# Performance work log

Measured on AMD Instinct MI355X. Metric: run time of the kernel, lower is better.

## Reference

```python
import jax, jax.numpy as jnp
import numpy as np


def setup_inputs() -> dict:
    key = jax.random.key(0)
    k1, k2 = jax.random.split(key)
    B, H, L = 8, 768, 4096
    x = jax.random.normal(k1, (B, H, L), dtype=jnp.float32)
    k = jax.random.normal(k2, (H, L), dtype=jnp.float32)
    return {"x": x, "k": k, "n": L}


def reference(x, k, n):
    # FFT-based long convolution: fft(x) * fft(k), inverse fft, real part,
    # truncated to the input sequence length. Inputs are real, so rfft/irfft
    # compute the identical result to complex fft + .real, at half the work.
    L = x.shape[-1]
    xf = jnp.fft.rfft(x, n=n)                 # [B, H, n//2+1] complex
    kf = jnp.fft.rfft(k, n=n)                 # [H, n//2+1]   complex
    y = jnp.fft.irfft(xf * kf, n=n)[..., :L]  # [B, H, L]
    return y.astype(x.dtype)
```

## Files before the change

### kernel.cpp

```cpp
#include <hip/hip_runtime.h>
#include <math.h>


#define NT 512
#define KF_LD 2049
#define C_SQRT1_2 0.70710678118654752f
#define INV_4096 2.44140625e-4f

#define SW(a) ((a) ^ (((a) >> 5) & 31) ^ (((a) >> 2) & 24))
__device__ __forceinline__ int WP(int a) {
  const int s = SW(a);
  return 2 * s - (s & 63);
}

__device__ __forceinline__ void sincos_rev(float f, float& sn, float& cs) {
  float s_, c_;
  asm("v_sin_f32 %0, %1" : "=v"(s_) : "v"(f));
  asm("v_cos_f32 %0, %1" : "=v"(c_) : "v"(f));
  sn = s_; cs = c_;
}

template <int SIGN>
__device__ __forceinline__ void bf8(const float ar[8], const float ai[8],
                                    float br[8], float bi[8]) {
  float s0r = ar[0] + ar[4], s0i = ai[0] + ai[4];
  float s1r = ar[0] - ar[4], s1i = ai[0] - ai[4];
  float s2r = ar[2] + ar[6], s2i = ai[2] + ai[6];
  float s3r = ar[2] - ar[6], s3i = ai[2] - ai[6];
  float E0r = s0r + s2r, E0i = s0i + s2i;
  float E2r = s0r - s2r, E2i = s0i - s2i;
  float E1r, E1i, E3r, E3i;
  if (SIGN < 0) { E1r = s1r + s3i; E1i = s1i - s3r; E3r = s1r - s3i; E3i = s1i + s3r; }
  else          { E1r = s1r - s3i; E1i = s1i + s3r; E3r = s1r + s3i; E3i = s1i - s3r; }
  float u0r = ar[1] + ar[5], u0i = ai[1] + ai[5];
  float u1r = ar[1] - ar[5], u1i = ai[1] - ai[5];
  float u2r = ar[3] + ar[7], u2i = ai[3] + ai[7];
  float u3r = ar[3] - ar[7], u3i = ai[3] - ai[7];
  float O0r = u0r + u2r, O0i = u0i + u2i;
  float O2r = u0r - u2r, O2i = u0i - u2i;
  float O1r, O1i, O3r, O3i;
  if (SIGN < 0) { O1r = u1r + u3i; O1i = u1i - u3r; O3r = u1r - u3i; O3i = u1i + u3r; }
  else          { O1r = u1r - u3i; O1i = u1i + u3r; O3r = u1r + u3i; O3i = u1i - u3r; }
  float t1r, t1i, t2r, t2i, t3r, t3i;
  if (SIGN < 0) {
    t1r = C_SQRT1_2 * (O1r + O1i); t1i = C_SQRT1_2 * (O1i - O1r);
    t2r = O2i;  t2i = -O2r;
    t3r = C_SQRT1_2 * (O3i - O3r); t3i = -C_SQRT1_2 * (O3r + O3i);
  } else {
    t1r = C_SQRT1_2 * (O1r - O1i); t1i = C_SQRT1_2 * (O1i + O1r);
    t2r = -O2i; t2i = O2r;
    t3r = -C_SQRT1_2 * (O3r + O3i); t3i = C_SQRT1_2 * (O3r - O3i);
  }
  br[0] = E0r + O0r; bi[0] = E0i + O0i;
  br[4] = E0r - O0r; bi[4] = E0i - O0i;
  br[1] = E1r + t1r; bi[1] = E1i + t1i;
  br[5] = E1r - t1r; bi[5] = E1i - t1i;
  br[2] = E2r + t2r; bi[2] = E2i + t2i;
  br[6] = E2r - t2r; bi[6] = E2i - t2i;
  br[3] = E3r + t3r; bi[3] = E3i + t3i;
  br[7] = E3r - t3r; bi[7] = E3i - t3i;
}

template <int SIGN, int S>
__device__ __forceinline__ void tw_write(float* Y, int ob,
                                         const float br[8], const float bi[8],
                                         float f1) {
  { const int i0 = WP(ob); Y[i0] = br[0]; Y[i0 + 64] = bi[0]; }
  float sn, cs;
  sincos_rev(f1, sn, cs);
  const float w1r = cs, w1i = (SIGN > 0) ? sn : -sn;
  float cwr = w1r, cwi = w1i;
#pragma unroll
  for (int m = 1; m < 8; ++m) {
    const int idx = WP(ob + S * m);
    Y[idx] = br[m] * cwr - bi[m] * cwi;
    Y[idx + 64] = br[m] * cwi + bi[m] * cwr;
    if (m < 7) {
      const float nr = cwr * w1r - cwi * w1i;
      const float ni = cwr * w1i + cwi * w1r;
      cwr = nr; cwi = ni;
    }
  }
}

template <int SIGN, int S>
__device__ __forceinline__ void stage_r8(const float* X, float* Y,
                                         const int rd[8]) {
  const int t = (int)threadIdx.x;
  const int q = t & (S - 1);
  const int p = t / S;
  float ar[8], ai[8];
#pragma unroll
  for (int j = 0; j < 8; ++j) {
    ar[j] = X[rd[j]];
    ai[j] = X[rd[j] + 64];
  }
  float br[8], bi[8];
  bf8<SIGN>(ar, ai, br, bi);
  tw_write<SIGN, S>(Y, q + 8 * S * p, br, bi, (float)(S * p) * INV_4096);
}

__device__ __forceinline__ void stage1_conv(const float* __restrict__ x0,
                                            const float* __restrict__ x1,
                                            float* Y) {
  const int t = (int)threadIdx.x;
  float ar[8], ai[8];
#pragma unroll
  for (int j = 0; j < 8; ++j) {
    ar[j] = x0[t + 512 * j];
    ai[j] = x1[t + 512 * j];
  }
  float br[8], bi[8];
  bf8<-1>(ar, ai, br, bi);
  tw_write<-1, 1>(Y, 8 * t, br, bi, (float)t * INV_4096);
}

__device__ __forceinline__ void stage4_kf(const float* X, float* Y,
                                          const float2* __restrict__ kfrow,
                                          const int rd[8]) {
  const int t = (int)threadIdx.x;
  float ar[8], ai[8];
#pragma unroll
  for (int j = 0; j < 8; ++j) {
    ar[j] = X[rd[j]];
    ai[j] = X[rd[j] + 64];
  }
  float br[8], bi[8];
  bf8<-1>(ar, ai, br, bi);
#pragma unroll
  for (int m = 0; m < 8; ++m) {
    const int k = t + 512 * m;
    float2 kv;
    if (m <= 3) {
      kv = kfrow[k];
    } else {
      kv = kfrow[4096 - k];
      kv.y = -kv.y;
    }
    const int i = WP(k);
    Y[i] = br[m] * kv.x - bi[m] * kv.y;
    Y[i + 64] = br[m] * kv.y + bi[m] * kv.x;
  }
}

__device__ __forceinline__ void stage4_store(const float* X,
                                             float* __restrict__ y0,
                                             float* __restrict__ y1,
                                             const int rd[8]) {
  const int t = (int)threadIdx.x;
  float ar[8], ai[8];
#pragma unroll
  for (int j = 0; j < 8; ++j) {
    ar[j] = X[rd[j]];
    ai[j] = X[rd[j] + 64];
  }
  float br[8], bi[8];
  bf8<1>(ar, ai, br, bi);
#pragma unroll
  for (int m = 0; m < 8; ++m) {
    const int k = t + 512 * m;
    y0[k] = br[m];
    y1[k] = bi[m];
  }
}

__device__ __forceinline__ void stage1_k(const float* __restrict__ kin,
                                         float* Y) {
  const int t = (int)threadIdx.x;
  float ar[8], ai[8];
#pragma unroll
  for (int j = 0; j < 8; ++j) {
    ar[j] = kin[t + 512 * j];
    ai[j] = 0.0f;
  }
  float br[8], bi[8];
  bf8<-1>(ar, ai, br, bi);
  tw_write<-1, 1>(Y, 8 * t, br, bi, (float)t * INV_4096);
}

__device__ __forceinline__ void stage4_kstore(const float* X,
                                              float2* __restrict__ kfrow,
                                              const int rd[8]) {
  const int t = (int)threadIdx.x;
  float ar[8], ai[8];
#pragma unroll
  for (int j = 0; j < 8; ++j) {
    ar[j] = X[rd[j]];
    ai[j] = X[rd[j] + 64];
  }
  float br[8], bi[8];
  bf8<-1>(ar, ai, br, bi);
  const float sc = 1.0f / 4096.0f;
#pragma unroll
  for (int m = 0; m < 4; ++m) {
    const int k = t + 512 * m;
    kfrow[k] = make_float2(br[m] * sc, bi[m] * sc);
  }
  if (t == 0) kfrow[2048] = make_float2(br[4] * sc, bi[4] * sc);
}

__global__ __launch_bounds__(NT) void kfft_kernel(const float* __restrict__ kin,
                                                  float2* __restrict__ kf) {
  __shared__ float A_[8192];
  __shared__ float B_[8192];
  const int t = (int)threadIdx.x;
  const int h = (int)blockIdx.x;
  int rd[8];
#pragma unroll
  for (int j = 0; j < 8; ++j) rd[j] = WP(t + 512 * j);
  stage1_k(kin + (size_t)h * 4096, A_);
  __syncthreads();
  stage_r8<-1, 8>(A_, B_, rd);
  __syncthreads();
  stage_r8<-1, 64>(B_, A_, rd);
  __syncthreads();
  stage4_kstore(A_, kf + (size_t)h * KF_LD, rd);
}

__global__ __launch_bounds__(NT) void conv_kernel(const float* __restrict__ x,
                                                  const float2* __restrict__ kf,
                                                  float* __restrict__ y, int H) {
  __shared__ float A_[8192];
  __shared__ float B_[8192];
  const int bi = (int)blockIdx.x;
  const int h = bi % H;
  const int j = bi / H;
  const size_t r0 = (size_t)(2 * j) * H + h;
  const size_t r1 = r0 + H;
  const float* src0 = x + r0 * 4096;
  const float* src1 = x + r1 * 4096;
  float* dst0 = y + r0 * 4096;
  float* dst1 = y + r1 * 4096;
  const float2* kfrow = kf + (size_t)h * KF_LD;
  const int t = (int)threadIdx.x;
  int rd[8];
#pragma unroll
  for (int jj = 0; jj < 8; ++jj) rd[jj] = WP(t + 512 * jj);
  stage1_conv(src0, src1, A_);
  __syncthreads();
  stage_r8<-1, 8>(A_, B_, rd);
  __syncthreads();
  stage_r8<-1, 64>(B_, A_, rd);
  __syncthreads();
  stage4_kf(A_, B_, kfrow, rd);
  __syncthreads();
  stage_r8<1, 1>(B_, A_, rd);
  __syncthreads();
  stage_r8<1, 8>(A_, B_, rd);
  __syncthreads();
  stage_r8<1, 64>(B_, A_, rd);
  __syncthreads();
  stage4_store(A_, dst0, dst1, rd);
}

extern "C" void kernel_launch(void* const* d_in, const int* in_sizes, int n_in,
                              void* d_out, int out_size, void* d_ws, size_t ws_size,
                              hipStream_t stream) {
  const float* x = (const float*)d_in[0];
  const float* kin = (const float*)d_in[1];
  float* y = (float*)d_out;
  const int H = in_sizes[1] / 4096;
  const int BH = in_sizes[0] / 4096;
  float2* kf = (float2*)d_ws;
  hipLaunchKernelGGL(kfft_kernel, dim3(H), dim3(NT), 0, stream, kin, kf);
  hipLaunchKernelGGL(conv_kernel, dim3(BH / 2), dim3(NT), 0, stream, x, kf, y, H);
}
```

Baseline: 62.74 us.

## Make conv blocks persistent over several pairs with register prefetch of next input

Each conv block now handles NPB=6 row pairs in sequence. While the current pair runs its FFT stages, the block prefetches the next pair's inputs into registers, so global load latency overlaps with shared-memory compute. The kernel-FFT kernel switches to a single in-place shared buffer with extra barriers, which cuts its LDS footprint. The cost is fewer blocks (pairs/6), extra register pressure, and a grid that truncates if the pair count is not divisible by 6.

Result: slower. 76.31 us (+21.6%).

```diff
diff --git a/kernel.cpp b/kernel.cpp
--- a/kernel.cpp
+++ b/kernel.cpp
@@ -3,6 +3,7 @@
 
 
 #define NT 512
+#define NPB 6
 #define KF_LD 2049
 #define C_SQRT1_2 0.70710678118654752f
 #define INV_4096 2.44140625e-4f
@@ -100,21 +101,6 @@
   tw_write<SIGN, S>(Y, q + 8 * S * p, br, bi, (float)(S * p) * INV_4096);
 }
 
-__device__ __forceinline__ void stage1_conv(const float* __restrict__ x0,
-                                            const float* __restrict__ x1,
-                                            float* Y) {
-  const int t = (int)threadIdx.x;
-  float ar[8], ai[8];
-#pragma unroll
-  for (int j = 0; j < 8; ++j) {
-    ar[j] = x0[t + 512 * j];
-    ai[j] = x1[t + 512 * j];
-  }
-  float br[8], bi[8];
-  bf8<-1>(ar, ai, br, bi);
-  tw_write<-1, 1>(Y, 8 * t, br, bi, (float)t * INV_4096);
-}
-
 __device__ __forceinline__ void stage4_kf(const float* X, float* Y,
                                           const float2* __restrict__ kfrow,
                                           const int rd[8]) {
@@ -137,7 +123,7 @@
       kv = kfrow[4096 - k];
       kv.y = -kv.y;
     }
-    const int i = WP(k);
+    const int i = rd[m];
     Y[i] = br[m] * kv.x - bi[m] * kv.y;
     Y[i + 64] = br[m] * kv.y + bi[m] * kv.x;
   }
@@ -164,93 +150,130 @@
   }
 }
 
-__device__ __forceinline__ void stage1_k(const float* __restrict__ kin,
-                                         float* Y) {
-  const int t = (int)threadIdx.x;
-  float ar[8], ai[8];
-#pragma unroll
-  for (int j = 0; j < 8; ++j) {
-    ar[j] = kin[t + 512 * j];
-    ai[j] = 0.0f;
-  }
+__device__ __forceinline__ void conv_pair(const float* __restrict__ x,
+                                          float* __restrict__ y,
+                                          const float2* __restrict__ kf,
+                                          int H, int p, int pmax,
+                                          float (&arC)[8], float (&aiC)[8],
+                                          float (&arN)[8], float (&aiN)[8],
+                                          float* A_, float* B_,
+                                          const int rd[8]) {
+  const int t = (int)threadIdx.x;
+  const int h = p % H, b2 = p / H;
+  const size_t r0 = ((size_t)(2 * b2) * H + (size_t)h) * 4096;
+  float* d0 = y + r0;
+  float* d1 = d0 + (size_t)H * 4096;
+  const float2* kfrow = kf + (size_t)h * KF_LD;
+  {
+    float br[8], bi[8];
+    bf8<-1>(arC, aiC, br, bi);
+    tw_write<-1, 1>(A_, 8 * t, br, bi, (float)t * INV_4096);
+  }
+  __syncthreads();
+  {
+    const int pn = (p + 1 < pmax) ? p + 1 : p;
+    const int hn = pn % H, bn = pn / H;
+    const float* s0 = x + ((size_t)(2 * bn) * H + (size_t)hn) * 4096;
+    const float* s1 = s0 + (size_t)H * 4096;
+#pragma unroll
+    for (int j = 0; j < 8; ++j) {
+      arN[j] = s0[t + 512 * j];
+      aiN[j] = s1[t + 512 * j];
+    }
+  }
+  stage_r8<-1, 8>(A_, B_, rd);   __syncthreads();
+  stage_r8<-1, 64>(B_, A_, rd);  __syncthreads();
+  stage4_kf(A_, B_, kfrow, rd);  __syncthreads();
+  stage_r8<1, 1>(B_, A_, rd);    __syncthreads();
+  stage_r8<1, 8>(A_, B_, rd);    __syncthreads();
+  stage_r8<1, 64>(B_, A_, rd);   __syncthreads();
+  stage4_store(A_, d0, d1, rd);
+  __syncthreads();
+}
+
+__device__ __forceinline__ void stage_r8_ip_k(float* Z, const int rd[8],
+                                              int S_, int dummy);
+template <int S>
+__device__ __forceinline__ void stage_r8_ip(float* Z, const int rd[8]) {
+  const int t = (int)threadIdx.x;
+  const int q = t & (S - 1);
+  const int p = t / S;
+  float ar[8], ai[8];
+#pragma unroll
+  for (int j = 0; j < 8; ++j) {
+    ar[j] = Z[rd[j]];
+    ai[j] = Z[rd[j] + 64];
+  }
+  __syncthreads();
   float br[8], bi[8];
   bf8<-1>(ar, ai, br, bi);
-  tw_write<-1, 1>(Y, 8 * t, br, bi, (float)t * INV_4096);
-}
-
-__device__ __forceinline__ void stage4_kstore(const float* X,
-                                              float2* __restrict__ kfrow,
-                                              const int rd[8]) {
-  const int t = (int)threadIdx.x;
-  float ar[8], ai[8];
-#pragma unroll
-  for (int j = 0; j < 8; ++j) {
-    ar[j] = X[rd[j]];
-    ai[j] = X[rd[j] + 64];
-  }
-  float br[8], bi[8];
-  bf8<-1>(ar, ai, br, bi);
-  const float sc = 1.0f / 4096.0f;
-#pragma unroll
-  for (int m = 0; m < 4; ++m) {
-    const int k = t + 512 * m;
-    kfrow[k] = make_float2(br[m] * sc, bi[m] * sc);
-  }
-  if (t == 0) kfrow[2048] = make_float2(br[4] * sc, bi[4] * sc);
+  tw_write<-1, S>(Z, q + 8 * S * p, br, bi, (float)(S * p) * INV_4096);
+  __syncthreads();
 }
 
 __global__ __launch_bounds__(NT) void kfft_kernel(const float* __restrict__ kin,
                                                   float2* __restrict__ kf) {
+  __shared__ float Z_[8192];
+  const int t = (int)threadIdx.x;
+  const int h = (int)blockIdx.x;
+  int rd[8];
+#pragma unroll
+  for (int j = 0; j < 8; ++j) rd[j] = WP(t + 512 * j);
+  {
+    const float* src = kin + (size_t)h * 4096;
+    float ar[8], ai[8];
+#pragma unroll
+    for (int j = 0; j < 8; ++j) { ar[j] = src[t + 512 * j]; ai[j] = 0.0f; }
+    float br[8], bi[8];
+    bf8<-1>(ar, ai, br, bi);
+    tw_write<-1, 1>(Z_, 8 * t, br, bi, (float)t * INV_4096);
+  }
+  __syncthreads();
+  stage_r8_ip<8>(Z_, rd);
+  stage_r8_ip<64>(Z_, rd);
+  {
+    float ar[8], ai[8];
+#pragma unroll
+    for (int j = 0; j < 8; ++j) { ar[j] = Z_[rd[j]]; ai[j] = Z_[rd[j] + 64]; }
+    float br[8], bi[8];
+    bf8<-1>(ar, ai, br, bi);
+    const float sc = 1.0f / 4096.0f;
+    float2* kfrow = kf + (size_t)h * KF_LD;
+#pragma unroll
+    for (int m = 0; m < 4; ++m) {
+      const int k = t + 512 * m;
+      kfrow[k] = make_float2(br[m] * sc, bi[m] * sc);
+    }
+    if (t == 0) kfrow[2048] = make_float2(br[4] * sc, bi[4] * sc);
+  }
+}
+
+__global__ __launch_bounds__(NT) void conv_kernel(const float* __restrict__ x,
+                                                  const float2* __restrict__ kf,
+                                                  float* __restrict__ y, int H,
+                                                  int pmax) {
   __shared__ float A_[8192];
   __shared__ float B_[8192];
   const int t = (int)threadIdx.x;
-  const int h = (int)blockIdx.x;
   int rd[8];
 #pragma unroll
   for (int j = 0; j < 8; ++j) rd[j] = WP(t + 512 * j);
-  stage1_k(kin + (size_t)h * 4096, A_);
-  __syncthreads();
-  stage_r8<-1, 8>(A_, B_, rd);
-  __syncthreads();
-  stage_r8<-1, 64>(B_, A_, rd);
-  __syncthreads();
-  stage4_kstore(A_, kf + (size_t)h * KF_LD, rd);
-}
-
-__global__ __launch_bounds__(NT) void conv_kernel(const float* __restrict__ x,
-                                                  const float2* __restrict__ kf,
-                                                  float* __restrict__ y, int H) {
-  __shared__ float A_[8192];
-  __shared__ float B_[8192];
-  const int bi = (int)blockIdx.x;
-  const int h = bi % H;
-  const int j = bi / H;
-  const size_t r0 = (size_t)(2 * j) * H + h;
-  const size_t r1 = r0 + H;
-  const float* src0 = x + r0 * 4096;
-  const float* src1 = x + r1 * 4096;
-  float* dst0 = y + r0 * 4096;
-  float* dst1 = y + r1 * 4096;
-  const float2* kfrow = kf + (size_t)h * KF_LD;
-  const int t = (int)threadIdx.x;
-  int rd[8];
-#pragma unroll
-  for (int jj = 0; jj < 8; ++jj) rd[jj] = WP(t + 512 * jj);
-  stage1_conv(src0, src1, A_);
-  __syncthreads();
-  stage_r8<-1, 8>(A_, B_, rd);
-  __syncthreads();
-  stage_r8<-1, 64>(B_, A_, rd);
-  __syncthreads();
-  stage4_kf(A_, B_, kfrow, rd);
-  __syncthreads();
-  stage_r8<1, 1>(B_, A_, rd);
-  __syncthreads();
-  stage_r8<1, 8>(A_, B_, rd);
-  __syncthreads();
-  stage_r8<1, 64>(B_, A_, rd);
-  __syncthreads();
-  stage4_store(A_, dst0, dst1, rd);
+  const int p0 = (int)blockIdx.x * NPB;
+  float arA[8], aiA[8], arB[8], aiB[8];
+  {
+    const int h = p0 % H, b2 = p0 / H;
+    const float* s0 = x + ((size_t)(2 * b2) * H + (size_t)h) * 4096;
+    const float* s1 = s0 + (size_t)H * 4096;
+#pragma unroll
+    for (int j = 0; j < 8; ++j) {
+      arA[j] = s0[t + 512 * j];
+      aiA[j] = s1[t + 512 * j];
+    }
+  }
+  for (int ii = 0; ii < NPB; ii += 2) {
+    conv_pair(x, y, kf, H, p0 + ii, pmax, arA, aiA, arB, aiB, A_, B_, rd);
+    conv_pair(x, y, kf, H, p0 + ii + 1, pmax, arB, aiB, arA, aiA, A_, B_, rd);
+  }
 }
 
 extern "C" void kernel_launch(void* const* d_in, const int* in_sizes, int n_in,
@@ -261,7 +284,10 @@
   float* y = (float*)d_out;
   const int H = in_sizes[1] / 4096;
   const int BH = in_sizes[0] / 4096;
+  const int pairs = BH / 2;
+  const int blocks = pairs / NPB;
   float2* kf = (float2*)d_ws;
   hipLaunchKernelGGL(kfft_kernel, dim3(H), dim3(NT), 0, stream, kin, kf);
-  hipLaunchKernelGGL(conv_kernel, dim3(BH / 2), dim3(NT), 0, stream, x, kf, y, H);
-}
+  hipLaunchKernelGGL(conv_kernel, dim3(blocks), dim3(NT), 0, stream, x, kf, y, H,
+                     pairs);
+}
```
